# Kernel optimization log

Hardware: AMD Instinct MI355X
Metric: run time of the kernel (lower is better)

## Reference

```python
import jax, jax.numpy as jnp
import numpy as np

EMBED_DIM = 1024
NUM_HEADS = 16
HEAD_DIM = EMBED_DIM // NUM_HEADS
B, T = 2, 2048


def setup_inputs() -> dict:
    key = jax.random.key(0)
    ks = jax.random.split(key, 10)
    s_in = 1.0 / np.sqrt(EMBED_DIM)
    s_hd = 1.0 / np.sqrt(HEAD_DIM)
    return {
        "hidden_states": jax.random.normal(ks[0], (B, T, EMBED_DIM), jnp.float32),
        "attn_mask": jnp.zeros((T, T), jnp.float32),
        # per-head parameter stacks (nn.Linear: y = x @ W^T + b); store W pre-transposed
        "W_q": jax.random.uniform(ks[1], (NUM_HEADS, EMBED_DIM, HEAD_DIM), jnp.float32, -s_in, s_in),
        "b_q": jax.random.uniform(ks[2], (NUM_HEADS, HEAD_DIM), jnp.float32, -s_in, s_in),
        "W_k": jax.random.uniform(ks[3], (NUM_HEADS, EMBED_DIM, HEAD_DIM), jnp.float32, -s_in, s_in),
        "b_k": jax.random.uniform(ks[4], (NUM_HEADS, HEAD_DIM), jnp.float32, -s_in, s_in),
        "W_v": jax.random.uniform(ks[5], (NUM_HEADS, EMBED_DIM, HEAD_DIM), jnp.float32, -s_in, s_in),
        "b_v": jax.random.uniform(ks[6], (NUM_HEADS, HEAD_DIM), jnp.float32, -s_in, s_in),
        "W_o": jax.random.uniform(ks[7], (NUM_HEADS, HEAD_DIM, EMBED_DIM), jnp.float32, -s_hd, s_hd),
        "b_o": jax.random.uniform(ks[8], (NUM_HEADS, EMBED_DIM), jnp.float32, -s_hd, s_hd),
        "gate": jnp.ones((NUM_HEADS,), jnp.float32),
    }


def reference(hidden_states, attn_mask, W_q, b_q, W_k, b_k, W_v, b_v, W_o, b_o, gate):
    # All heads: state='active', consent=True (defaults); dropout in eval mode.
    scale = 1.0 / np.sqrt(HEAD_DIM)
    # Q,K,V: [B,H,T,hd]
    Q = jnp.einsum("btd,hde->bhte", hidden_states, W_q) + b_q[None, :, None, :]
    K = jnp.einsum("btd,hde->bhte", hidden_states, W_k) + b_k[None, :, None, :]
    V = jnp.einsum("btd,hde->bhte", hidden_states, W_v) + b_v[None, :, None, :]
    scores = jnp.einsum("bhte,bhse->bhts", Q, K) * scale + attn_mask[None, None, :, :]
    weights = jax.nn.softmax(scores, axis=-1)
    out = jnp.einsum("bhts,bhse->bhte", weights, V)  # [B,H,T,hd]
    # per-head scalar norm: mean over (B,T) of L2 norm along head_dim, floored at 1e-5
    denom = jnp.maximum(
        jnp.sqrt(jnp.sum(out * out, axis=-1)).mean(axis=(0, 2)), 1e-5
    )  # [H]
    out_n = out / denom[None, :, None, None]
    g = jnp.clip(gate, 0.0, 1.0)  # gate_factor = 1.0 for 'active' heads
    # projected per head: (out_n @ W_o + b_o) * g; then sum over heads / H
    proj = (jnp.einsum("bhte,hed->bhtd", out_n, W_o) + b_o[None, :, None, :]) * g[None, :, None, None]
    return proj.sum(axis=1) / NUM_HEADS
```

## Files before the change

### kernel.cpp

```cpp
#include <hip/hip_runtime.h>
#include <hip/hip_bf16.h>
#include <math.h>

#define EMBED_DIM 1024
#define NUM_HEADS 16
#define HEAD_DIM  64
#define B_SZ      2
#define T_SZ      2048
#define BT        (B_SZ * T_SZ)
#define LOG2E     1.44269504088896340736f
#define QSCALE    (0.125f * LOG2E)
#define SOFT_OFF  8.0f

typedef short bf16x8 __attribute__((ext_vector_type(8)));
typedef float f32x4  __attribute__((ext_vector_type(4)));

#define MFMA16(a, b, c) __builtin_amdgcn_mfma_f32_16x16x32_bf16((a), (b), (c), 0, 0, 0)

__device__ inline short f2bf(float f) {
    unsigned u = __builtin_bit_cast(unsigned, f);
    u = (u + 0x7fffu + ((u >> 16) & 1u)) >> 16;
    return (short)u;
}
__device__ inline float bf2f(short s) {
    unsigned u = ((unsigned)(unsigned short)s) << 16;
    return __builtin_bit_cast(float, u);
}
__device__ inline unsigned pk2(float a, float b) {
#if __has_builtin(__builtin_amdgcn_cvt_pk_bf16_f32)
    typedef __bf16 bf2_t __attribute__((ext_vector_type(2)));
    bf2_t t = __builtin_amdgcn_cvt_pk_bf16_f32(a, b);
    return __builtin_bit_cast(unsigned, t);
#else
    return (unsigned)(unsigned short)f2bf(a) | ((unsigned)(unsigned short)f2bf(b) << 16);
#endif
}

__device__ inline float ex2(float x) {
#if __has_builtin(__builtin_amdgcn_exp2f)
    return __builtin_amdgcn_exp2f(x);
#else
    return exp2f(x);
#endif
}

__device__ inline void gld16(const short* g, short* lds) {
    __builtin_amdgcn_global_load_lds(
        (const __attribute__((address_space(1))) void*)g,
        (__attribute__((address_space(3))) void*)lds, 16, 0, 0);
}

__device__ inline bf16x8 frag_swz(const short* tile, int R, int C) {
    return *(const bf16x8*)(tile + R * 64 + ((C ^ (R & 7)) << 3));
}

__device__ inline float red_add64(float v) {
    v += __shfl_xor(v, 1); v += __shfl_xor(v, 2); v += __shfl_xor(v, 4);
    v += __shfl_xor(v, 8); v += __shfl_xor(v, 16); v += __shfl_xor(v, 32);
    return v;
}

__global__ __launch_bounds__(256) void prep_kernel(
    const float* __restrict__ hs, short* __restrict__ hsb,
    const float* __restrict__ maskf, unsigned* __restrict__ flagsW,
    const float* __restrict__ Wq, const float* __restrict__ Wk,
    const float* __restrict__ Wv, const float* __restrict__ Wo,
    short* __restrict__ Wqt, short* __restrict__ Wkt,
    short* __restrict__ Wvt, short* __restrict__ Wo2)
{
    __shared__ float tile[32][33];
    const int bx = blockIdx.x, tid = threadIdx.x;

    if (bx < 4096) {
        const long i = ((long)bx * 256 + tid) * 4;
        const float4 v = *(const float4*)(hs + i);
        ushort4 o; o.x = f2bf(v.x); o.y = f2bf(v.y); o.z = f2bf(v.z); o.w = f2bf(v.w);
        *(ushort4*)(hsb + i) = o;
    } else if (bx < 4608) {
        const int flat = bx - 4096;
        const int qc = flat >> 5, kt = flat & 31;
        const float* base = maskf + (long)qc * 128 * 2048 + kt * 64;
        unsigned u = 0;
        #pragma unroll
        for (int i = 0; i < 8; ++i) {
            const int f2 = i * 256 + tid;
            const int r = f2 >> 4, c4 = f2 & 15;
            const uint4 v = *(const uint4*)(base + (long)r * 2048 + c4 * 4);
            u |= v.x | v.y | v.z | v.w;
        }
        if (__any(u != 0) && (tid & 63) == 0)
            atomicOr(&flagsW[qc], 1u << kt);
    } else {
        const int j = bx - 4608;
        const int x = j & 63, rest = j >> 6;
        const int h = rest & 15, arr = rest >> 4;
        const float* src; short* dst; int C;
        if (arr == 0)      { src = Wq; dst = Wqt; C = 64; }
        else if (arr == 1) { src = Wk; dst = Wkt; C = 64; }
        else if (arr == 2) { src = Wv; dst = Wvt; C = 64; }
        else               { src = Wo; dst = Wo2; C = 1024; }
        src += (long)h * 65536;
        if (arr != 3) dst += (long)h * 65536;

        const int ct = C / 32;
        const int tr = x / ct, tc = x % ct;
        const int tx = tid & 31, ty = tid >> 5;
        #pragma unroll
        for (int i = 0; i < 4; ++i) {
            const int r = ty + 8 * i;
            tile[r][tx] = src[(long)(tr * 32 + r) * C + tc * 32 + tx];
        }
        __syncthreads();
        #pragma unroll
        for (int i = 0; i < 4; ++i) {
            const int r = ty + 8 * i;
            if (arr == 3)
                dst[(long)(tc * 32 + r) * 1024 + h * 64 + tr * 32 + tx] = f2bf(tile[tx][r]);
            else
                dst[(long)(tc * 32 + r) * 1024 + tr * 32 + tx] = f2bf(tile[tx][r]);
        }
    }
}

__global__ __launch_bounds__(256) void qkv_mfma_kernel(
    const short* __restrict__ hsb,
    const short* __restrict__ Wt,
    const float* __restrict__ bq, const float* __restrict__ bk,
    const float* __restrict__ bv,
    short* __restrict__ Qb, short* __restrict__ Kb, short* __restrict__ Vtb)
{
    const int r_ = blockIdx.x;
    const int c_ = r_ & 7, j_ = r_ >> 3;
    const int xi = j_ & 7, yi = j_ >> 3;
    const int m0 = ((c_ & 3) * 8 + xi) * 128;
    const int n0 = ((c_ >> 2) * 12 + yi) * 128;
    const int type = n0 >> 10;

    __shared__ short As[128 * 64];
    __shared__ short Bs[128 * 64];

    const int tid = threadIdx.x, lane = tid & 63, w = tid >> 6;
    const int wm = w & 1, wn = w >> 1;
    const int quad = lane >> 4, l15 = lane & 15;

    f32x4 acc[4][4] = {};

    if (type < 2) {
        for (int k0 = 0; k0 < 1024; k0 += 64) {
            __syncthreads();
            #pragma unroll
            for (int t = 0; t < 4; ++t) {
                const int r0 = w * 32 + t * 8;
                const int r  = r0 + (lane >> 3);
                const int cg = (lane & 7) ^ (r & 7);
                gld16(hsb + (long)(m0 + r) * 1024 + k0 + cg * 8, &As[r0 * 64]);
                gld16(Wt  + (long)(n0 + r) * 1024 + k0 + cg * 8, &Bs[r0 * 64]);
            }
            __syncthreads();
            #pragma unroll
            for (int ks = 0; ks < 2; ++ks) {
                bf16x8 af[4];
                #pragma unroll
                for (int ms = 0; ms < 4; ++ms)
                    af[ms] = frag_swz(As, wm * 64 + ms * 16 + l15, ks * 4 + quad);
                #pragma unroll
                for (int ns = 0; ns < 4; ++ns) {
                    const bf16x8 bfr = frag_swz(Bs, wn * 64 + ns * 16 + l15, ks * 4 + quad);
                    #pragma unroll
                    for (int ms = 0; ms < 4; ++ms)
                        acc[ms][ns] = MFMA16(bfr, af[ms], acc[ms][ns]);
                }
            }
        }

        const int hh = (((n0 + wn * 64) >> 6) & 15);
        const float* bsrc = (type == 0 ? bq : bk) + hh * 64;
        short* dst = (type == 0 ? Qb : Kb);
        const float sc = (type == 0) ? QSCALE : 1.0f;
        #pragma unroll
        for (int ns = 0; ns < 4; ++ns) {
            const int e0 = ns * 16 + quad * 4;
            const float4 b4 = *(const float4*)(bsrc + e0);
            #pragma unroll
            for (int ms = 0; ms < 4; ++ms) {
                const int t  = m0 + wm * 64 + ms * 16 + l15;
                const int bb = t >> 11, t0 = t & 2047;
                ushort4 pk;
                pk.x = (unsigned short)f2bf((acc[ms][ns][0] + b4.x) * sc);
                pk.y = (unsigned short)f2bf((acc[ms][ns][1] + b4.y) * sc);
                pk.z = (unsigned short)f2bf((acc[ms][ns][2] + b4.z) * sc);
                pk.w = (unsigned short)f2bf((acc[ms][ns][3] + b4.w) * sc);
                *(ushort4*)&dst[((long)(bb * 16 + hh) * 2048 + t0) * 64 + e0] = pk;
            }
        }
    } else {
        for (int k0 = 0; k0 < 1024; k0 += 64) {
            __syncthreads();
            #pragma unroll
            for (int t = 0; t < 4; ++t) {
                const int r0 = w * 32 + t * 8;
                const int r  = r0 + (lane >> 3);
                const int cg = (lane & 7) ^ (r & 7);
                gld16(hsb + (long)(m0 + r) * 1024 + k0 + cg * 8, &As[r0 * 64]);
                gld16(Wt  + (long)(n0 + r) * 1024 + k0 + cg * 8, &Bs[r0 * 64]);
            }
            __syncthreads();
            #pragma unroll
            for (int ks = 0; ks < 2; ++ks) {
                bf16x8 af[4];
                #pragma unroll
                for (int ms = 0; ms < 4; ++ms)
                    af[ms] = frag_swz(As, wm * 64 + ms * 16 + l15, ks * 4 + quad);
                #pragma unroll
                for (int ns = 0; ns < 4; ++ns) {
                    const bf16x8 bfr = frag_swz(Bs, wn * 64 + ns * 16 + l15, ks * 4 + quad);
                    #pragma unroll
                    for (int ms = 0; ms < 4; ++ms)
                        acc[ms][ns] = MFMA16(af[ms], bfr, acc[ms][ns]);
                }
            }
        }

        #pragma unroll
        for (int ns = 0; ns < 4; ++ns) {
            const int n = n0 + wn * 64 + ns * 16 + l15;
            const int h = (n >> 6) & 15;
            const int e = n & 63;
            const float bias = bv[h * 64 + e];
            #pragma unroll
            for (int ms = 0; ms < 4; ++ms) {
                const int mbase = m0 + wm * 64 + ms * 16 + quad * 4;
                const int bb = mbase >> 11, t0 = mbase & 2047;
                const int tp = (t0 & ~63) | (t0 & 35) | ((t0 & 12) << 1) | ((t0 & 16) >> 2);
                ushort4 pk;
                pk.x = (unsigned short)f2bf(acc[ms][ns][0] + bias);
                pk.y = (unsigned short)f2bf(acc[ms][ns][1] + bias);
                pk.z = (unsigned short)f2bf(acc[ms][ns][2] + bias);
                pk.w = (unsigned short)f2bf(acc[ms][ns][3] + bias);
                *(ushort4*)&Vtb[((long)(bb * 16 + h) * 64 + e) * 2048 + tp] = pk;
            }
        }
    }
}

__global__ __launch_bounds__(512) void attn_mfma_kernel(
    const short* __restrict__ Qb, const short* __restrict__ Kb,
    const short* __restrict__ Vtb, const float* __restrict__ maskf,
    const unsigned* __restrict__ flagsW,
    short* __restrict__ Ob, float* __restrict__ denomsum)
{
    const int r_  = blockIdx.x;
    const int c_  = r_ & 7, j_ = r_ >> 3;
    const int g_  = c_ + 8 * (j_ >> 4);
    const int qc  = j_ & 15;
    const int q0  = qc * 128;
    const int h   = g_ & 15, b = g_ >> 4;
    const long bh = ((long)b * 16 + h) * (long)T_SZ * 64;

    __shared__ short Ks[2][128 * 64];
    __shared__ short Vs[2][128 * 64];
    __shared__ float wred[8];

    const int tid = threadIdx.x, lane = tid & 63, w = tid >> 6;
    const int quad = lane >> 4, l15 = lane & 15;
    const int qrow = q0 + w * 16 + l15;

    const unsigned zf = flagsW[qc];

    const short* Kg = Kb + bh;
    const short* Vg = Vtb + bh;

    bf16x8 qf[2];
    #pragma unroll
    for (int ks = 0; ks < 2; ++ks)
        qf[ks] = *(const bf16x8*)(Qb + bh + (long)qrow * 64 + ks * 32 + quad * 8);

    bf16x8 ones;
    #pragma unroll
    for (int i = 0; i < 8; ++i) ones[i] = (short)0x3F80;

    f32x4 o[4] = {};
    f32x4 lacc = {};

    const float* mrow = maskf + (long)qrow * 2048 + quad * 4;

    auto stageKV = [&](int st, int buf) {
        const int kv0 = st * 128;
        #pragma unroll
        for (int t = 0; t < 2; ++t) {
            const int r0 = w * 16 + t * 8;
            const int r  = r0 + (lane >> 3);
            const int cg = (lane & 7) ^ (r & 7);
            gld16(Kg + (long)(kv0 + r) * 64 + cg * 8, &Ks[buf][r0 * 64]);
        }
        #pragma unroll
        for (int t = 0; t < 2; ++t) {
            const int r0 = w * 8;
            const int r  = r0 + (lane >> 3);
            const int cg = (lane & 7) ^ (r & 7);
            gld16(Vg + (long)r * 2048 + kv0 + t * 64 + cg * 8,
                  &Vs[buf][t * 4096 + r0 * 64]);
        }
    };

    stageKV(0, 0);

    for (int st = 0; st < 16; ++st) {
        const int cur = st & 1;

        __builtin_amdgcn_s_barrier();
        asm volatile("" ::: "memory");
        if (st < 15) {
            stageKV(st + 1, cur ^ 1);
            asm volatile("s_waitcnt vmcnt(4)" ::: "memory");
        } else {
            asm volatile("s_waitcnt vmcnt(0)" ::: "memory");
        }
        __builtin_amdgcn_s_barrier();
        asm volatile("" ::: "memory");

        #pragma unroll
        for (int k2 = 0; k2 < 2; ++k2) {
            const int kt = st * 2 + k2;
            const short* Kt = &Ks[cur][k2 * 4096];
            const short* Vt = &Vs[cur][k2 * 4096];

            f32x4 s[4];
            if (zf & (1u << kt)) {
                const int kv0 = kt * 64;
                #pragma unroll
                for (int kb = 0; kb < 4; ++kb) {
                    const float4 m = *(const float4*)(mrow + kv0 + kb * 16);
                    s[kb][0] = fmaf(m.x, LOG2E, -SOFT_OFF);
                    s[kb][1] = fmaf(m.y, LOG2E, -SOFT_OFF);
                    s[kb][2] = fmaf(m.z, LOG2E, -SOFT_OFF);
                    s[kb][3] = fmaf(m.w, LOG2E, -SOFT_OFF);
                }
            } else {
                #pragma unroll
                for (int kb = 0; kb < 4; ++kb) {
                    s[kb][0] = -SOFT_OFF; s[kb][1] = -SOFT_OFF;
                    s[kb][2] = -SOFT_OFF; s[kb][3] = -SOFT_OFF;
                }
            }

            __builtin_amdgcn_s_setprio(1);
            #pragma unroll
            for (int ks = 0; ks < 2; ++ks)
                #pragma unroll
                for (int kb = 0; kb < 4; ++kb) {
                    const bf16x8 kf = frag_swz(Kt, kb * 16 + l15, ks * 4 + quad);
                    s[kb] = MFMA16(kf, qf[ks], s[kb]);
                }
            __builtin_amdgcn_s_setprio(0);

            unsigned w0[4], w1[4];
            #pragma unroll
            for (int kb = 0; kb < 4; ++kb) {
                const float p0 = ex2(s[kb][0]);
                const float p1 = ex2(s[kb][1]);
                const float p2 = ex2(s[kb][2]);
                const float p3 = ex2(s[kb][3]);
                w0[kb] = pk2(p0, p1);
                w1[kb] = pk2(p2, p3);
            }

            __builtin_amdgcn_s_setprio(1);
            #pragma unroll
            for (int kbp = 0; kbp < 2; ++kbp) {
                const uint4 u = {w0[2 * kbp], w1[2 * kbp],
                                 w0[2 * kbp + 1], w1[2 * kbp + 1]};
                const bf16x8 pb = __builtin_bit_cast(bf16x8, u);
                lacc = MFMA16(ones, pb, lacc);
                #pragma unroll
                for (int eb = 0; eb < 4; ++eb) {
                    const bf16x8 va = frag_swz(Vt, eb * 16 + l15, kbp * 4 + quad);
                    o[eb] = MFMA16(va, pb, o[eb]);
                }
            }
            __builtin_amdgcn_s_setprio(0);
        }
    }

    const float inv = 1.f / lacc[0];
    float ss = 0.f;
    #pragma unroll
    for (int eb = 0; eb < 4; ++eb) {
        o[eb] *= inv;
        #pragma unroll
        for (int r = 0; r < 4; ++r) ss += o[eb][r] * o[eb][r];
    }
    ss += __shfl_xor(ss, 16);
    ss += __shfl_xor(ss, 32);
    const float tot = sqrtf(ss);

    #pragma unroll
    for (int eb = 0; eb < 4; ++eb) {
        uint2 pk;
        pk.x = pk2(o[eb][0], o[eb][1]);
        pk.y = pk2(o[eb][2], o[eb][3]);
        *(uint2*)&Ob[((long)(b * 2048 + qrow)) * 1024 + h * 64 + eb * 16 + quad * 4] = pk;
    }

    const float wsum = red_add64(tot) * 0.25f;
    if (lane == 0) wred[w] = wsum;
    __syncthreads();
    if (tid == 0) {
        float acc = 0.f;
        #pragma unroll
        for (int i = 0; i < 8; ++i) acc += wred[i];
        atomicAdd(&denomsum[h], acc);
    }
}

__global__ __launch_bounds__(256) void oproj_mfma_kernel(
    const short* __restrict__ Ob,
    const short* __restrict__ Wo2,
    const float* __restrict__ bo,
    const float* __restrict__ gate,
    const float* __restrict__ denomsum,
    float* __restrict__ out)
{
    const int m0 = blockIdx.x * 128;
    const int n0 = blockIdx.y * 64;
    __shared__ short As[128 * 64];
    __shared__ short Bs[64 * 64];
    __shared__ float sh_s[16], sh_g[16];

    const int tid = threadIdx.x, lane = tid & 63, w = tid >> 6;
    const int wm = w & 1, wn = w >> 1;
    const int quad = lane >> 4, l15 = lane & 15;

    if (tid < 16) {
        const float g  = fminf(fmaxf(gate[tid], 0.f), 1.f);
        const float dn = fmaxf(denomsum[tid] * (1.f / (float)BT), 1e-5f);
        sh_g[tid] = g * (1.f / (float)NUM_HEADS);
        sh_s[tid] = g / (dn * (float)NUM_HEADS);
    }

    f32x4 acc[4][2] = {};

    for (int k0 = 0; k0 < 1024; k0 += 64) {
        const int hh = k0 >> 6;
        __syncthreads();
        #pragma unroll
        for (int t = 0; t < 4; ++t) {
            const int r0 = w * 32 + t * 8;
            const int r  = r0 + (lane >> 3);
            const int cg = (lane & 7) ^ (r & 7);
            gld16(Ob + (long)(m0 + r) * 1024 + k0 + cg * 8, &As[r0 * 64]);
        }
        #pragma unroll
        for (int t = 0; t < 2; ++t) {
            const int r0 = w * 16 + t * 8;
            const int r  = r0 + (lane >> 3);
            const int cg = (lane & 7) ^ (r & 7);
            gld16(Wo2 + (long)(n0 + r) * 1024 + k0 + cg * 8, &Bs[r0 * 64]);
        }
        __syncthreads();

        f32x4 sacc[4][2] = {};
        #pragma unroll
        for (int ks = 0; ks < 2; ++ks) {
            bf16x8 af[4];
            #pragma unroll
            for (int ms = 0; ms < 4; ++ms)
                af[ms] = frag_swz(As, wm * 64 + ms * 16 + l15, ks * 4 + quad);
            #pragma unroll
            for (int ns = 0; ns < 2; ++ns) {
                const bf16x8 bfr = frag_swz(Bs, wn * 32 + ns * 16 + l15, ks * 4 + quad);
                #pragma unroll
                for (int ms = 0; ms < 4; ++ms)
                    sacc[ms][ns] = MFMA16(af[ms], bfr, sacc[ms][ns]);
            }
        }
        const float sc = sh_s[hh];
        #pragma unroll
        for (int ms = 0; ms < 4; ++ms)
            #pragma unroll
            for (int ns = 0; ns < 2; ++ns)
                acc[ms][ns] += sacc[ms][ns] * sc;
    }

    #pragma unroll
    for (int ns = 0; ns < 2; ++ns) {
        const int n = n0 + wn * 32 + ns * 16 + l15;
        float be = 0.f;
        #pragma unroll
        for (int hh = 0; hh < 16; ++hh) be += sh_g[hh] * bo[hh * 1024 + n];
        #pragma unroll
        for (int ms = 0; ms < 4; ++ms) {
            const int m = m0 + wm * 64 + ms * 16 + quad * 4;
            #pragma unroll
            for (int r = 0; r < 4; ++r)
                out[(long)(m + r) * 1024 + n] = acc[ms][ns][r] + be;
        }
    }
}

extern "C" void kernel_launch(void* const* d_in, const int* in_sizes, int n_in,
                              void* d_out, int out_size, void* d_ws, size_t ws_size,
                              hipStream_t stream)
{
    const float* hs   = (const float*)d_in[0];
    const float* mask = (const float*)d_in[1];
    const float* Wq   = (const float*)d_in[2];
    const float* bq   = (const float*)d_in[3];
    const float* Wk   = (const float*)d_in[4];
    const float* bk   = (const float*)d_in[5];
    const float* Wv   = (const float*)d_in[6];
    const float* bv   = (const float*)d_in[7];
    const float* Wo   = (const float*)d_in[8];
    const float* bo   = (const float*)d_in[9];
    const float* gate = (const float*)d_in[10];
    float* out = (float*)d_out;

    char* ws = (char*)d_ws;
    const size_t MB = 1024 * 1024;
    short* hsb   = (short*)(ws);
    short* Wqt   = (short*)(ws + 8  * MB);
    short* Wkt   = (short*)(ws + 10 * MB);
    short* Wvt   = (short*)(ws + 12 * MB);
    short* Wo2   = (short*)(ws + 14 * MB);
    short* Qb    = (short*)(ws + 16 * MB);
    short* Kb    = (short*)(ws + 24 * MB);
    short* Vtb   = (short*)(ws + 32 * MB);
    short* Ob    = (short*)(ws + 40 * MB);
    float* denomsum = (float*)(ws + 48 * MB);
    unsigned* flagsW = (unsigned*)(ws + 48 * MB + 4096);

    (void)hipMemsetAsync(denomsum, 0, NUM_HEADS * sizeof(float), stream);
    (void)hipMemsetAsync(flagsW, 0, 16 * sizeof(unsigned), stream);

    prep_kernel<<<8704, 256, 0, stream>>>(
        hs, hsb, mask, flagsW, Wq, Wk, Wv, Wo, Wqt, Wkt, Wvt, Wo2);
    qkv_mfma_kernel<<<768, 256, 0, stream>>>(
        hsb, Wqt, bq, bk, bv, Qb, Kb, Vtb);
    attn_mfma_kernel<<<512, 512, 0, stream>>>(
        Qb, Kb, Vtb, mask, flagsW, Ob, denomsum);
    oproj_mfma_kernel<<<dim3(32, 16), 256, 0, stream>>>(
        Ob, Wo2, bo, gate, denomsum, out);
}
```

Measured before the change: 220.1 us.

## Use 4-wave attention blocks with two Q subtiles per wave and 64-key stages

Restructures the attention kernel from 8 waves of 16 query rows each to 4 waves of 32 query rows each, using two Q subtiles per wave. Each K and V fragment read from LDS now feeds two MFMA chains, halving LDS fragment traffic per FLOP. KV staging shrinks to 64-key tiles over 32 iterations, which cuts shared memory to allow more blocks per CU, at the cost of more barriers and higher register pressure. The two host memsets are also merged into one covering both the denominator sums and the flags.

```diff
diff --git a/kernel.cpp b/kernel.cpp
--- a/kernel.cpp
+++ b/kernel.cpp
@@ -243,7 +243,7 @@
     }
 }
 
-__global__ __launch_bounds__(512) void attn_mfma_kernel(
+__global__ __launch_bounds__(256, 4) void attn_mfma_kernel(
     const short* __restrict__ Qb, const short* __restrict__ Kb,
     const short* __restrict__ Vtb, const float* __restrict__ maskf,
     const unsigned* __restrict__ flagsW,
@@ -257,61 +257,57 @@
     const int h   = g_ & 15, b = g_ >> 4;
     const long bh = ((long)b * 16 + h) * (long)T_SZ * 64;
 
-    __shared__ short Ks[2][128 * 64];
-    __shared__ short Vs[2][128 * 64];
-    __shared__ float wred[8];
+    __shared__ short Ks[2][64 * 64];
+    __shared__ short Vs[2][64 * 64];
+    __shared__ float wred[4];
 
     const int tid = threadIdx.x, lane = tid & 63, w = tid >> 6;
     const int quad = lane >> 4, l15 = lane & 15;
-    const int qrow = q0 + w * 16 + l15;
+    const int qrowA = q0 + w * 32 + l15;
 
     const unsigned zf = flagsW[qc];
 
     const short* Kg = Kb + bh;
     const short* Vg = Vtb + bh;
 
-    bf16x8 qf[2];
+    bf16x8 qf[2][2];
     #pragma unroll
-    for (int ks = 0; ks < 2; ++ks)
-        qf[ks] = *(const bf16x8*)(Qb + bh + (long)qrow * 64 + ks * 32 + quad * 8);
+    for (int qs = 0; qs < 2; ++qs)
+        #pragma unroll
+        for (int ks = 0; ks < 2; ++ks)
+            qf[qs][ks] = *(const bf16x8*)(Qb + bh +
+                (long)(qrowA + qs * 16) * 64 + ks * 32 + quad * 8);
 
     bf16x8 ones;
     #pragma unroll
     for (int i = 0; i < 8; ++i) ones[i] = (short)0x3F80;
 
-    f32x4 o[4] = {};
-    f32x4 lacc = {};
-
-    const float* mrow = maskf + (long)qrow * 2048 + quad * 4;
-
-    auto stageKV = [&](int st, int buf) {
-        const int kv0 = st * 128;
+    f32x4 o[2][4] = {};
+    f32x4 lacc[2] = {};
+
+    const float* mrowA = maskf + (long)qrowA * 2048 + quad * 4;
+
+    auto stageKV = [&](int kt, int buf) {
+        const int kv0 = kt * 64;
         #pragma unroll
         for (int t = 0; t < 2; ++t) {
             const int r0 = w * 16 + t * 8;
             const int r  = r0 + (lane >> 3);
             const int cg = (lane & 7) ^ (r & 7);
             gld16(Kg + (long)(kv0 + r) * 64 + cg * 8, &Ks[buf][r0 * 64]);
-        }
-        #pragma unroll
-        for (int t = 0; t < 2; ++t) {
-            const int r0 = w * 8;
-            const int r  = r0 + (lane >> 3);
-            const int cg = (lane & 7) ^ (r & 7);
-            gld16(Vg + (long)r * 2048 + kv0 + t * 64 + cg * 8,
-                  &Vs[buf][t * 4096 + r0 * 64]);
+            gld16(Vg + (long)r * 2048 + kv0 + cg * 8, &Vs[buf][r0 * 64]);
         }
     };
 
     stageKV(0, 0);
 
-    for (int st = 0; st < 16; ++st) {
-        const int cur = st & 1;
+    for (int kt = 0; kt < 32; ++kt) {
+        const int cur = kt & 1;
 
         __builtin_amdgcn_s_barrier();
         asm volatile("" ::: "memory");
-        if (st < 15) {
-            stageKV(st + 1, cur ^ 1);
+        if (kt < 31) {
+            stageKV(kt + 1, cur ^ 1);
             asm volatile("s_waitcnt vmcnt(4)" ::: "memory");
         } else {
             asm volatile("s_waitcnt vmcnt(0)" ::: "memory");
@@ -319,98 +315,113 @@
         __builtin_amdgcn_s_barrier();
         asm volatile("" ::: "memory");
 
-        #pragma unroll
-        for (int k2 = 0; k2 < 2; ++k2) {
-            const int kt = st * 2 + k2;
-            const short* Kt = &Ks[cur][k2 * 4096];
-            const short* Vt = &Vs[cur][k2 * 4096];
-
-            f32x4 s[4];
-            if (zf & (1u << kt)) {
-                const int kv0 = kt * 64;
+        f32x4 s[2][4];
+        if (zf & (1u << kt)) {
+            const int kv0 = kt * 64;
+            #pragma unroll
+            for (int qs = 0; qs < 2; ++qs)
                 #pragma unroll
                 for (int kb = 0; kb < 4; ++kb) {
-                    const float4 m = *(const float4*)(mrow + kv0 + kb * 16);
-                    s[kb][0] = fmaf(m.x, LOG2E, -SOFT_OFF);
-                    s[kb][1] = fmaf(m.y, LOG2E, -SOFT_OFF);
-                    s[kb][2] = fmaf(m.z, LOG2E, -SOFT_OFF);
-                    s[kb][3] = fmaf(m.w, LOG2E, -SOFT_OFF);
+                    const float4 m = *(const float4*)(mrowA +
+                        (long)qs * 16 * 2048 + kv0 + kb * 16);
+                    s[qs][kb][0] = fmaf(m.x, LOG2E, -SOFT_OFF);
+                    s[qs][kb][1] = fmaf(m.y, LOG2E, -SOFT_OFF);
+                    s[qs][kb][2] = fmaf(m.z, LOG2E, -SOFT_OFF);
+                    s[qs][kb][3] = fmaf(m.w, LOG2E, -SOFT_OFF);
                 }
-            } else {
+        } else {
+            #pragma unroll
+            for (int qs = 0; qs < 2; ++qs)
                 #pragma unroll
                 for (int kb = 0; kb < 4; ++kb) {
-                    s[kb][0] = -SOFT_OFF; s[kb][1] = -SOFT_OFF;
-                    s[kb][2] = -SOFT_OFF; s[kb][3] = -SOFT_OFF;
+                    s[qs][kb][0] = -SOFT_OFF; s[qs][kb][1] = -SOFT_OFF;
+                    s[qs][kb][2] = -SOFT_OFF; s[qs][kb][3] = -SOFT_OFF;
                 }
-            }
-
-            __builtin_amdgcn_s_setprio(1);
+        }
+
+        bf16x8 kf[2][4];
+        #pragma unroll
+        for (int ks = 0; ks < 2; ++ks)
+            #pragma unroll
+            for (int kb = 0; kb < 4; ++kb)
+                kf[ks][kb] = frag_swz(&Ks[cur][0], kb * 16 + l15, ks * 4 + quad);
+
+        __builtin_amdgcn_s_setprio(1);
+        #pragma unroll
+        for (int qs = 0; qs < 2; ++qs)
             #pragma unroll
             for (int ks = 0; ks < 2; ++ks)
                 #pragma unroll
-                for (int kb = 0; kb < 4; ++kb) {
-                    const bf16x8 kf = frag_swz(Kt, kb * 16 + l15, ks * 4 + quad);
-                    s[kb] = MFMA16(kf, qf[ks], s[kb]);
-                }
-            __builtin_amdgcn_s_setprio(0);
-
-            unsigned w0[4], w1[4];
+                for (int kb = 0; kb < 4; ++kb)
+                    s[qs][kb] = MFMA16(kf[ks][kb], qf[qs][ks], s[qs][kb]);
+        __builtin_amdgcn_s_setprio(0);
+
+        unsigned w0[2][4], w1[2][4];
+        #pragma unroll
+        for (int qs = 0; qs < 2; ++qs)
             #pragma unroll
             for (int kb = 0; kb < 4; ++kb) {
-                const float p0 = ex2(s[kb][0]);
-                const float p1 = ex2(s[kb][1]);
-                const float p2 = ex2(s[kb][2]);
-                const float p3 = ex2(s[kb][3]);
-                w0[kb] = pk2(p0, p1);
-                w1[kb] = pk2(p2, p3);
-            }
-
-            __builtin_amdgcn_s_setprio(1);
+                const float p0 = ex2(s[qs][kb][0]);
+                const float p1 = ex2(s[qs][kb][1]);
+                const float p2 = ex2(s[qs][kb][2]);
+                const float p3 = ex2(s[qs][kb][3]);
+                w0[qs][kb] = pk2(p0, p1);
+                w1[qs][kb] = pk2(p2, p3);
+            }
+
+        bf16x8 va[2][4];
+        #pragma unroll
+        for (int kbp = 0; kbp < 2; ++kbp)
+            #pragma unroll
+            for (int eb = 0; eb < 4; ++eb)
+                va[kbp][eb] = frag_swz(&Vs[cur][0], eb * 16 + l15, kbp * 4 + quad);
+
+        __builtin_amdgcn_s_setprio(1);
+        #pragma unroll
+        for (int qs = 0; qs < 2; ++qs)
             #pragma unroll
             for (int kbp = 0; kbp < 2; ++kbp) {
-                const uint4 u = {w0[2 * kbp], w1[2 * kbp],
-                                 w0[2 * kbp + 1], w1[2 * kbp + 1]};
+                const uint4 u = {w0[qs][2 * kbp], w1[qs][2 * kbp],
+                                 w0[qs][2 * kbp + 1], w1[qs][2 * kbp + 1]};
                 const bf16x8 pb = __builtin_bit_cast(bf16x8, u);
-                lacc = MFMA16(ones, pb, lacc);
-                #pragma unroll
-                for (int eb = 0; eb < 4; ++eb) {
-                    const bf16x8 va = frag_swz(Vt, eb * 16 + l15, kbp * 4 + quad);
-                    o[eb] = MFMA16(va, pb, o[eb]);
-                }
-            }
-            __builtin_amdgcn_s_setprio(0);
-        }
-    }
-
-    const float inv = 1.f / lacc[0];
-    float ss = 0.f;
+                lacc[qs] = MFMA16(ones, pb, lacc[qs]);
+                #pragma unroll
+                for (int eb = 0; eb < 4; ++eb)
+                    o[qs][eb] = MFMA16(va[kbp][eb], pb, o[qs][eb]);
+            }
+        __builtin_amdgcn_s_setprio(0);
+    }
+
+    float tot = 0.f;
     #pragma unroll
-    for (int eb = 0; eb < 4; ++eb) {
-        o[eb] *= inv;
-        #pragma unroll
-        for (int r = 0; r < 4; ++r) ss += o[eb][r] * o[eb][r];
-    }
-    ss += __shfl_xor(ss, 16);
-    ss += __shfl_xor(ss, 32);
-    const float tot = sqrtf(ss);
-
-    #pragma unroll
-    for (int eb = 0; eb < 4; ++eb) {
-        uint2 pk;
-        pk.x = pk2(o[eb][0], o[eb][1]);
-        pk.y = pk2(o[eb][2], o[eb][3]);
-        *(uint2*)&Ob[((long)(b * 2048 + qrow)) * 1024 + h * 64 + eb * 16 + quad * 4] = pk;
+    for (int qs = 0; qs < 2; ++qs) {
+        const float inv = 1.f / lacc[qs][0];
+        float ss = 0.f;
+        #pragma unroll
+        for (int eb = 0; eb < 4; ++eb) {
+            o[qs][eb] *= inv;
+            #pragma unroll
+            for (int r = 0; r < 4; ++r) ss += o[qs][eb][r] * o[qs][eb][r];
+        }
+        ss += __shfl_xor(ss, 16);
+        ss += __shfl_xor(ss, 32);
+        tot += sqrtf(ss);
+
+        const int qrow = qrowA + qs * 16;
+        #pragma unroll
+        for (int eb = 0; eb < 4; ++eb) {
+            uint2 pk;
+            pk.x = pk2(o[qs][eb][0], o[qs][eb][1]);
+            pk.y = pk2(o[qs][eb][2], o[qs][eb][3]);
+            *(uint2*)&Ob[((long)(b * 2048 + qrow)) * 1024 + h * 64 + eb * 16 + quad * 4] = pk;
+        }
     }
 
     const float wsum = red_add64(tot) * 0.25f;
     if (lane == 0) wred[w] = wsum;
     __syncthreads();
-    if (tid == 0) {
-        float acc = 0.f;
-        #pragma unroll
-        for (int i = 0; i < 8; ++i) acc += wred[i];
-        atomicAdd(&denomsum[h], acc);
-    }
+    if (tid == 0)
+        atomicAdd(&denomsum[h], wred[0] + wred[1] + wred[2] + wred[3]);
 }
 
 __global__ __launch_bounds__(256) void oproj_mfma_kernel(
@@ -527,16 +538,15 @@
     short* Vtb   = (short*)(ws + 32 * MB);
     short* Ob    = (short*)(ws + 40 * MB);
     float* denomsum = (float*)(ws + 48 * MB);
-    unsigned* flagsW = (unsigned*)(ws + 48 * MB + 4096);
-
-    (void)hipMemsetAsync(denomsum, 0, NUM_HEADS * sizeof(float), stream);
-    (void)hipMemsetAsync(flagsW, 0, 16 * sizeof(unsigned), stream);
+    unsigned* flagsW = (unsigned*)(ws + 48 * MB + 64);
+
+    (void)hipMemsetAsync(denomsum, 0, 128, stream);
 
     prep_kernel<<<8704, 256, 0, stream>>>(
         hs, hsb, mask, flagsW, Wq, Wk, Wv, Wo, Wqt, Wkt, Wvt, Wo2);
     qkv_mfma_kernel<<<768, 256, 0, stream>>>(
         hsb, Wqt, bq, bk, bv, Qb, Kb, Vtb);
-    attn_mfma_kernel<<<512, 512, 0, stream>>>(
+    attn_mfma_kernel<<<512, 256, 0, stream>>>(
         Qb, Kb, Vtb, mask, flagsW, Ob, denomsum);
     oproj_mfma_kernel<<<dim3(32, 16), 256, 0, stream>>>(
         Ob, Wo2, bo, gate, denomsum, out);
```

New measurement: 241.6 us. 1.1x slower.
